# Kernel tuning notes

Measured on AMD Instinct MI355X. Metric: run time of the kernel, lower is better.

The kernel has to match this reference:

```python
import jax, jax.numpy as jnp
import numpy as np

B, N, E = 128, 50000, 1600000


def setup_inputs() -> dict:
    key = jax.random.key(0)
    k1, k2, k3, k4, k5 = jax.random.split(key, 5)
    x = jax.random.normal(k1, (B, N), dtype=jnp.float32)
    h = jax.random.normal(k2, (N,), dtype=jnp.float32)
    J = jax.random.normal(k3, (E,), dtype=jnp.float32)
    edge_idx_i = jax.random.randint(k4, (E,), 0, N, dtype=jnp.int64) if jax.config.jax_enable_x64 else jax.random.randint(k4, (E,), 0, N, dtype=jnp.int32)
    edge_idx_j = jax.random.randint(k5, (E,), 0, N, dtype=jnp.int32)
    return {"x": x, "h": h, "J": J, "edge_idx_i": edge_idx_i, "edge_idx_j": edge_idx_j}


def reference(x, h, J, edge_idx_i, edge_idx_j):
    # Hamiltonian: H(x) = x @ h + (x[:, ei] * x[:, ej]) @ J  -> shape (B,)
    interactions = x[:, edge_idx_i] * x[:, edge_idx_j]  # (B, E)
    return x @ h + interactions @ J
```

## Files before the change

### kernel.cpp

```cpp
#include <hip/hip_runtime.h>
#include <hip/hip_bf16.h>
#include <hip/hip_fp16.h>

#define BDIM    128
#define NGROUPS 4
#define GCOLS   32
#define ROWB    (GCOLS * 2)
#define EBLK    2048
#define RANKS   (EBLK / NGROUPS)
#define WPG     (RANKS * 4)
#define S1BLK   (NGROUPS * 8)
#define HBLK2   8
#define RPS     (RANKS / 8)

__global__ __launch_bounds__(256) void transpose_h_kernel(
    const float* __restrict__ x, const float* __restrict__ h,
    __half* __restrict__ xTh, float* __restrict__ hp, int N) {
  __shared__ float tile[64][BDIM + 1];
  __shared__ float sh[64];
  __shared__ float red2[2][BDIM];
  const int tid = threadIdx.x;
  const int n0  = blockIdx.x * 64;

  const int tn  = tid & 63;
  const int tb0 = tid >> 6;
  const int n   = n0 + tn;
  if (n < N) {
    for (int b = tb0; b < BDIM; b += 4) tile[tn][b] = x[(size_t)b * N + n];
  } else {
    for (int b = tb0; b < BDIM; b += 4) tile[tn][b] = 0.f;
  }
  if (tid < 64) sh[tid] = (n0 + tid < N) ? h[n0 + tid] : 0.f;
  __syncthreads();

  const int hb   = tid & 127;
  const int half = tid >> 7;
  float hacc = 0.f;
#pragma unroll
  for (int m = 0; m < 32; ++m) {
    const int nl = half * 32 + m;
    hacc += tile[nl][hb] * sh[nl];
  }
  red2[half][hb] = hacc;

  const int c2 = tid & 15;
  const int g2 = (tid >> 4) & 3;
  const int k  = tid >> 6;
  for (int it = 0; it < 16; ++it) {
    const int nl = it * 4 + k;
    if (n0 + nl < N) {
      const float a = tile[nl][g2 * GCOLS + 2 * c2];
      const float b = tile[nl][g2 * GCOLS + 2 * c2 + 1];
      __half2* dst = (__half2*)(xTh + ((size_t)g2 * N + (n0 + nl)) * GCOLS + 2 * c2);
      *dst = __floats2half2_rn(a, b);
    }
  }
  __syncthreads();
  if (tid < BDIM) hp[(size_t)blockIdx.x * BDIM + tid] = red2[0][tid] + red2[1][tid];
}

__device__ __forceinline__ void fma8(float* acc, int4 vi, int4 vj, float Jv) {
  const int wi[4] = {vi.x, vi.y, vi.z, vi.w};
  const int wj[4] = {vj.x, vj.y, vj.z, vj.w};
#pragma unroll
  for (int w = 0; w < 4; ++w) {
    const __half2 hi = __builtin_bit_cast(__half2, wi[w]);
    const __half2 hj = __builtin_bit_cast(__half2, wj[w]);
    const __half2 p  = __hmul2(hi, hj);
    acc[2 * w]     += __low2float(p)  * Jv;
    acc[2 * w + 1] += __high2float(p) * Jv;
  }
}

__global__ __launch_bounds__(256, 8) void edge_kernel(
    const __half* __restrict__ xTh, const float* __restrict__ J,
    const int* __restrict__ ei, const int* __restrict__ ej,
    float* __restrict__ partials, int E, int N, int edges_per_wave) {
  const int tid  = threadIdx.x;
  const int g    = (blockIdx.x & 7) >> 1;
  const int rank = (blockIdx.x >> 3) * 2 + (blockIdx.x & 1);
  const int wave = tid >> 6;
  const int lane = tid & 63;
  const int k    = lane >> 2;
  const char* xgl = (const char*)xTh + (size_t)g * N * ROWB + (lane & 3) * 16;

  const int ws = (rank * 4 + wave) * edges_per_wave;
  const int we = min(ws + edges_per_wave, E);

  float acc[8] = {0.f, 0.f, 0.f, 0.f, 0.f, 0.f, 0.f, 0.f};

  int e0 = (ws < E) ? ws : E;
  for (; e0 + 32 <= we; e0 += 32) {
    const int eA = e0 + k;
    const int eB = eA + 16;
    const int   iA = ei[eA];
    const int   jA = ej[eA];
    const float JA = J[eA];
    const int   iB = ei[eB];
    const int   jB = ej[eB];
    const float JB = J[eB];
    const int4 viA = *(const int4*)(xgl + (unsigned)iA * ROWB);
    const int4 vjA = *(const int4*)(xgl + (unsigned)jA * ROWB);
    const int4 viB = *(const int4*)(xgl + (unsigned)iB * ROWB);
    const int4 vjB = *(const int4*)(xgl + (unsigned)jB * ROWB);
    fma8(acc, viA, vjA, JA);
    fma8(acc, viB, vjB, JB);
  }
  for (; e0 < we; e0 += 16) {
    const int e = e0 + k;
    int i = 0, j = 0;
    float Jv = 0.f;
    if (e < we) { i = ei[e]; j = ej[e]; Jv = J[e]; }
    const int4 vi = *(const int4*)(xgl + (unsigned)i * ROWB);
    const int4 vj = *(const int4*)(xgl + (unsigned)j * ROWB);
    fma8(acc, vi, vj, Jv);
  }

#pragma unroll
  for (int off = 4; off < 64; off <<= 1)
#pragma unroll
    for (int w = 0; w < 8; ++w) acc[w] += __shfl_xor(acc[w], off);

  __shared__ float red[4][GCOLS];
  if (lane < 4)
#pragma unroll
    for (int w = 0; w < 8; ++w) red[wave][(lane & 3) * 8 + w] = acc[w];
  __syncthreads();
  if (tid < GCOLS) {
    const float s = red[0][tid] + red[1][tid] + red[2][tid] + red[3][tid];
    partials[((size_t)g * RANKS + rank) * GCOLS + tid] = s;
  }
}

__global__ __launch_bounds__(256) void reduce1_kernel(
    const float* __restrict__ P, const float* __restrict__ hp,
    float* __restrict__ P2, float* __restrict__ hp2, int hrows) {
  __shared__ float red[8][GCOLS];
  __shared__ float redh[2][BDIM];
  if (blockIdx.x < S1BLK) {
    const int g  = blockIdx.x >> 3;
    const int s  = blockIdx.x & 7;
    const int rl = threadIdx.x >> 5;
    const int c  = threadIdx.x & 31;
    float acc = 0.f;
    for (int rr = rl; rr < RPS; rr += 8)
      acc += P[((size_t)g * RANKS + s * RPS + rr) * GCOLS + c];
    red[rl][c] = acc;
    __syncthreads();
    if (threadIdx.x < GCOLS) {
      float sum = 0.f;
      for (int r = 0; r < 8; ++r) sum += red[r][threadIdx.x];
      P2[(size_t)blockIdx.x * GCOLS + threadIdx.x] = sum;
    }
  } else {
    const int s  = blockIdx.x - S1BLK;
    const int b  = threadIdx.x & 127;
    const int rg = threadIdx.x >> 7;
    float acc = 0.f;
    for (int r = s + 8 * rg; r < hrows; r += 16)
      acc += hp[(size_t)r * BDIM + b];
    redh[rg][b] = acc;
    __syncthreads();
    if (threadIdx.x < BDIM)
      hp2[(size_t)s * BDIM + threadIdx.x] = redh[0][threadIdx.x] + redh[1][threadIdx.x];
  }
}

__global__ __launch_bounds__(128) void reduce2_kernel(
    const float* __restrict__ P2, const float* __restrict__ hp2,
    float* __restrict__ out) {
  const int b = threadIdx.x;
  const int g = b >> 5;
  const int c = b & 31;
  float acc = 0.f;
  for (int s = 0; s < 8; ++s) acc += hp2[(size_t)s * BDIM + b];
  for (int s = 0; s < 8; ++s) acc += P2[(size_t)(g * 8 + s) * GCOLS + c];
  out[b] = acc;
}

extern "C" void kernel_launch(void* const* d_in, const int* in_sizes, int n_in,
                              void* d_out, int out_size, void* d_ws, size_t ws_size,
                              hipStream_t stream) {
  const float* x  = (const float*)d_in[0];
  const float* h  = (const float*)d_in[1];
  const float* J  = (const float*)d_in[2];
  const int*   ei = (const int*)d_in[3];
  const int*   ej = (const int*)d_in[4];
  float* out = (float*)d_out;

  const int N = in_sizes[1];
  const int E = in_sizes[2];

  const int tblocks = (N + 63) / 64;

  __half* xTh = (__half*)d_ws;
  float* P   = (float*)(xTh + (size_t)NGROUPS * N * GCOLS);
  float* P2  = P   + (size_t)EBLK * GCOLS;
  float* hp  = P2  + (size_t)S1BLK * GCOLS;
  float* hp2 = hp  + (size_t)tblocks * BDIM;

  transpose_h_kernel<<<tblocks, 256, 0, stream>>>(x, h, xTh, hp, N);

  const int epw = (((E + WPG - 1) / WPG) + 31) & ~31;
  edge_kernel<<<EBLK, 256, 0, stream>>>(xTh, J, ei, ej, P, E, N, epw);

  reduce1_kernel<<<S1BLK + HBLK2, 256, 0, stream>>>(P, hp, P2, hp2, tblocks);

  reduce2_kernel<<<1, BDIM, 0, stream>>>(P2, hp2, out);
}
```

Measured before the change: 95.66 us.

## Software-pipeline edge gathers with double buffering and interleaved edge chunks

Rewrites the edge kernel loop as a two-stage software pipeline: the indices for the next chunk are loaded and the x rows for the following chunk are gathered while the current chunk's products are accumulated, with sched_barrier keeping the compiler from undoing the order. Waves now take 32-edge chunks in an interleaved stride across all waves instead of contiguous ranges, and tail edges are handled by clamping indices and zeroing J. Occupancy hint drops from 8 to 6 waves per SIMD so the extra live registers fit. The cost is higher register pressure and fewer resident waves, which lowers latency hiding through occupancy.

Result: slower. 97.71 us (+2.1%).

```diff
diff --git a/kernel.cpp b/kernel.cpp
--- a/kernel.cpp
+++ b/kernel.cpp
@@ -72,10 +72,10 @@
   }
 }
 
-__global__ __launch_bounds__(256, 8) void edge_kernel(
+__global__ __launch_bounds__(256, 6) void edge_kernel(
     const __half* __restrict__ xTh, const float* __restrict__ J,
     const int* __restrict__ ei, const int* __restrict__ ej,
-    float* __restrict__ partials, int E, int N, int edges_per_wave) {
+    float* __restrict__ partials, int E, int N) {
   const int tid  = threadIdx.x;
   const int g    = (blockIdx.x & 7) >> 1;
   const int rank = (blockIdx.x >> 3) * 2 + (blockIdx.x & 1);
@@ -84,37 +84,74 @@
   const int k    = lane >> 2;
   const char* xgl = (const char*)xTh + (size_t)g * N * ROWB + (lane & 3) * 16;
 
-  const int ws = (rank * 4 + wave) * edges_per_wave;
-  const int we = min(ws + edges_per_wave, E);
+  const int gw = rank * 4 + wave;
+  const int Tg = (E + 31) >> 5;
+  const int ns = (gw < Tg) ? (Tg - gw + WPG - 1) / WPG : 0;
+
+#define LOAD_IDX(sstep, iA, jA, JA, iB, jB, JB)                     \
+  do {                                                              \
+    const int e0_ = (gw + (sstep) * WPG) * 32;                      \
+    const int eA_ = e0_ + k, eB_ = eA_ + 16;                        \
+    const int eAc_ = min(eA_, E - 1), eBc_ = min(eB_, E - 1);       \
+    iA = ei[eAc_]; jA = ej[eAc_];                                   \
+    JA = (eA_ < E) ? J[eAc_] : 0.f;                                 \
+    iB = ei[eBc_]; jB = ej[eBc_];                                   \
+    JB = (eB_ < E) ? J[eBc_] : 0.f;                                 \
+  } while (0)
+
+#define GATHER(vA, wA, vB, wB, iA, jA, iB, jB)                      \
+  do {                                                              \
+    vA = *(const int4*)(xgl + (unsigned)(iA) * ROWB);               \
+    wA = *(const int4*)(xgl + (unsigned)(jA) * ROWB);               \
+    vB = *(const int4*)(xgl + (unsigned)(iB) * ROWB);               \
+    wB = *(const int4*)(xgl + (unsigned)(jB) * ROWB);               \
+  } while (0)
 
   float acc[8] = {0.f, 0.f, 0.f, 0.f, 0.f, 0.f, 0.f, 0.f};
 
-  int e0 = (ws < E) ? ws : E;
-  for (; e0 + 32 <= we; e0 += 32) {
-    const int eA = e0 + k;
-    const int eB = eA + 16;
-    const int   iA = ei[eA];
-    const int   jA = ej[eA];
-    const float JA = J[eA];
-    const int   iB = ei[eB];
-    const int   jB = ej[eB];
-    const float JB = J[eB];
-    const int4 viA = *(const int4*)(xgl + (unsigned)iA * ROWB);
-    const int4 vjA = *(const int4*)(xgl + (unsigned)jA * ROWB);
-    const int4 viB = *(const int4*)(xgl + (unsigned)iB * ROWB);
-    const int4 vjB = *(const int4*)(xgl + (unsigned)jB * ROWB);
-    fma8(acc, viA, vjA, JA);
-    fma8(acc, viB, vjB, JB);
-  }
-  for (; e0 < we; e0 += 16) {
-    const int e = e0 + k;
-    int i = 0, j = 0;
-    float Jv = 0.f;
-    if (e < we) { i = ei[e]; j = ej[e]; Jv = J[e]; }
-    const int4 vi = *(const int4*)(xgl + (unsigned)i * ROWB);
-    const int4 vj = *(const int4*)(xgl + (unsigned)j * ROWB);
-    fma8(acc, vi, vj, Jv);
-  }
+  int   iA0, jA0, iB0, jB0, iA1, jA1, iB1, jB1;
+  float JA0, JB0, JA1, JB1;
+  float JhA0, JhB0, JhA1, JhB1;
+  int4  viA0, vjA0, viB0, vjB0, viA1, vjA1, viB1, vjB1;
+
+  int s = 0;
+  if (ns > 0) {
+    LOAD_IDX(0, iA0, jA0, JA0, iB0, jB0, JB0);
+    GATHER(viA0, vjA0, viB0, vjB0, iA0, jA0, iB0, jB0);
+    JhA0 = JA0; JhB0 = JB0;
+    {
+      const int s1 = (ns > 1) ? 1 : 0;
+      LOAD_IDX(s1, iA1, jA1, JA1, iB1, jB1, JB1);
+    }
+
+    for (; s + 2 <= ns; s += 2) {
+      GATHER(viA1, vjA1, viB1, vjB1, iA1, jA1, iB1, jB1);
+      JhA1 = JA1; JhB1 = JB1;
+      {
+        const int s2 = min(s + 2, ns - 1);
+        LOAD_IDX(s2, iA0, jA0, JA0, iB0, jB0, JB0);
+      }
+      __builtin_amdgcn_sched_barrier(0);
+      fma8(acc, viA0, vjA0, JhA0);
+      fma8(acc, viB0, vjB0, JhB0);
+
+      GATHER(viA0, vjA0, viB0, vjB0, iA0, jA0, iB0, jB0);
+      JhA0 = JA0; JhB0 = JB0;
+      {
+        const int s3 = min(s + 3, ns - 1);
+        LOAD_IDX(s3, iA1, jA1, JA1, iB1, jB1, JB1);
+      }
+      __builtin_amdgcn_sched_barrier(0);
+      fma8(acc, viA1, vjA1, JhA1);
+      fma8(acc, viB1, vjB1, JhB1);
+    }
+    if (s < ns) {
+      fma8(acc, viA0, vjA0, JhA0);
+      fma8(acc, viB0, vjB0, JhB0);
+    }
+  }
+#undef LOAD_IDX
+#undef GATHER
 
 #pragma unroll
   for (int off = 4; off < 64; off <<= 1)
@@ -127,8 +164,8 @@
     for (int w = 0; w < 8; ++w) red[wave][(lane & 3) * 8 + w] = acc[w];
   __syncthreads();
   if (tid < GCOLS) {
-    const float s = red[0][tid] + red[1][tid] + red[2][tid] + red[3][tid];
-    partials[((size_t)g * RANKS + rank) * GCOLS + tid] = s;
+    const float sum = red[0][tid] + red[1][tid] + red[2][tid] + red[3][tid];
+    partials[((size_t)g * RANKS + rank) * GCOLS + tid] = sum;
   }
 }
 
@@ -201,8 +238,7 @@
 
   transpose_h_kernel<<<tblocks, 256, 0, stream>>>(x, h, xTh, hp, N);
 
-  const int epw = (((E + WPG - 1) / WPG) + 31) & ~31;
-  edge_kernel<<<EBLK, 256, 0, stream>>>(xTh, J, ei, ej, P, E, N, epw);
+  edge_kernel<<<EBLK, 256, 0, stream>>>(xTh, J, ei, ej, P, E, N);
 
   reduce1_kernel<<<S1BLK + HBLK2, 256, 0, stream>>>(P, hp, P2, hp2, tblocks);
 
```
